# Kernel optimization log

Measured on AMD Instinct MI355X. Metric: run time of the kernel, lower is better.

The kernel has to match this reference:

```python
import jax, jax.numpy as jnp
import numpy as np

B, S, D, H = 2, 2048, 1024, 16
HD = D // H  # 64


def setup_inputs() -> dict:
    key = jax.random.key(0)
    ks = jax.random.split(key, 11)
    w_scale = 1.0 / np.sqrt(D)
    Q = jax.random.normal(ks[0], (B, S, D), jnp.float32)
    K = jax.random.normal(ks[1], (B, S, D), jnp.float32)
    V = jax.random.normal(ks[2], (B, S, D), jnp.float32)
    # causal mask: True = masked (matches torch masked_fill semantics)
    mask = ~jnp.tril(jnp.ones((S, S), bool))[None, None]  # [1,1,S,S]
    # RoPE freqs (precomputed cos/sin of freqs_cis, shape [S, HD//2])
    inv_freq = 1.0 / (10000.0 ** (jnp.arange(0, HD, 2, dtype=jnp.float32) / HD))
    angles = jnp.arange(S, dtype=jnp.float32)[:, None] * inv_freq[None, :]
    freqs_cos, freqs_sin = jnp.cos(angles), jnp.sin(angles)
    wq = jax.random.normal(ks[3], (D, D), jnp.float32) * w_scale
    wk = jax.random.normal(ks[4], (D, D), jnp.float32) * w_scale
    wv = jax.random.normal(ks[5], (D, D), jnp.float32) * w_scale
    wo = jax.random.normal(ks[6], (D, D), jnp.float32) * w_scale
    bq = jax.random.normal(ks[7], (D,), jnp.float32) * 0.01
    bk = jax.random.normal(ks[8], (D,), jnp.float32) * 0.01
    bv = jax.random.normal(ks[9], (D,), jnp.float32) * 0.01
    bo = jax.random.normal(ks[10], (D,), jnp.float32) * 0.01
    return {"Q": Q, "K": K, "V": V, "mask": mask,
            "freqs_cos": freqs_cos, "freqs_sin": freqs_sin,
            "wq": wq, "bq": bq, "wk": wk, "bk": bk,
            "wv": wv, "bv": bv, "wo": wo, "bo": bo}


def _rope(x, cos, sin):
    # x: [B,S,H,HD]; complex pairing of adjacent dims as in view_as_complex
    xr, xi = x[..., 0::2], x[..., 1::2]
    c = cos[None, :, None, :]
    s = sin[None, :, None, :]
    out_r = xr * c - xi * s
    out_i = xr * s + xi * c
    return jnp.stack([out_r, out_i], axis=-1).reshape(x.shape)


def reference(Q, K, V, mask, freqs_cos, freqs_sin, wq, bq, wk, bk, wv, bv, wo, bo):
    b, s, d = Q.shape
    h = H
    hd = d // h
    q = (Q @ wq.T + bq).reshape(b, s, h, hd)
    k = (K @ wk.T + bk).reshape(b, s, h, hd)
    v = (V @ wv.T + bv).reshape(b, s, h, hd)
    q = _rope(q, freqs_cos, freqs_sin)
    k = _rope(k, freqs_cos, freqs_sin)
    q = q.transpose(0, 2, 1, 3)  # [B,H,S,HD]
    k = k.transpose(0, 2, 1, 3)
    v = v.transpose(0, 2, 1, 3)
    scale = jnp.sqrt(jnp.float32(hd))
    energy = jnp.einsum('bhqd,bhkd->bhqk', q, k) / scale
    energy = jnp.where(mask, jnp.float32(-1e10), energy)
    attn = jax.nn.softmax(energy, axis=-1)  # dropout p=0.0 -> identity
    out = jnp.einsum('bhqk,bhkd->bhqd', attn, v)
    out = out.transpose(0, 2, 1, 3).reshape(b, s, d)
    return out @ wo.T + bo
```

## Files before the change

kernel.cpp:

```cpp
#include <hip/hip_runtime.h>
#include <stdint.h>

#define NB 2
#define NS 2048
#define ND 1024
#define NH 16
#define NHD 64
#define NM (NB*NS)

typedef __bf16 bf16;
typedef float f32x4 __attribute__((ext_vector_type(4)));
typedef __bf16 bf16x8 __attribute__((ext_vector_type(8)));
typedef __bf16 bf16x4 __attribute__((ext_vector_type(4)));

#define MFMA16(a,b,c) __builtin_amdgcn_mfma_f32_16x16x32_bf16(a,b,c,0,0,0)

__device__ __forceinline__ void gld_lds16(const bf16* g, bf16* l) {
  __builtin_amdgcn_global_load_lds((const __attribute__((address_space(1))) void*)g,
                                   (__attribute__((address_space(3))) void*)l,
                                   16, 0, 0);
}

__device__ __forceinline__ void block_sync_lds() {
  asm volatile("s_waitcnt lgkmcnt(0)\n\ts_barrier" ::: "memory");
}

__global__ __launch_bounds__(256)
void cvt3(const float* __restrict__ s0, const float* __restrict__ s1,
          const float* __restrict__ s2, bf16* __restrict__ dst, int n4each) {
  const int t = blockIdx.y;
  const float* s = (t == 0) ? s0 : (t == 1) ? s1 : s2;
  int i = blockIdx.x * blockDim.x + threadIdx.x;
  if (i >= n4each) return;
  float4 v = ((const float4*)s)[i];
  bf16x4 o = { (bf16)v.x, (bf16)v.y, (bf16)v.z, (bf16)v.w };
  ((bf16x4*)(dst + (size_t)t * n4each * 4))[i] = o;
}

__global__ __launch_bounds__(256)
void cvt_w4(const float* __restrict__ s0, const float* __restrict__ s1,
            const float* __restrict__ s2, const float* __restrict__ s3,
            bf16* __restrict__ dst, int n4each) {
  const int t = blockIdx.y;
  const float* s = (t == 0) ? s0 : (t == 1) ? s1 : (t == 2) ? s2 : s3;
  int i = blockIdx.x * blockDim.x + threadIdx.x;
  if (i >= n4each) return;
  float4 v = ((const float4*)s)[i];
  bf16x4 o = { (bf16)v.x, (bf16)v.y, (bf16)v.z, (bf16)v.w };
  ((bf16x4*)(dst + (size_t)t * n4each * 4))[i] = o;
}

template<int MODE>
__global__ __launch_bounds__(256)
void gemm_nt(const bf16* __restrict__ A, const bf16* __restrict__ W,
             const float* __restrict__ b0, const float* __restrict__ b1,
             const float* __restrict__ b2,
             const float* __restrict__ fc, const float* __restrict__ fs,
             bf16* __restrict__ obf, bf16* __restrict__ vtp,
             float* __restrict__ of) {
  constexpr int K = ND;
  constexpr int BN = (MODE == 0) ? 128 : 64;
  constexpr int NJ = (MODE == 0) ? 4 : 2;
  constexpr int ITB = (MODE == 0) ? 4 : 2;
  __shared__ __align__(16) bf16 As[128 * 64];
  __shared__ __align__(16) bf16 Bs[BN * 64];
  const int tid = threadIdx.x;
  const int w = tid >> 6, lane = tid & 63;

  const int id = blockIdx.x;
  const int xcd = id & 7, r = id >> 3;
  int t, nt, mt;
  if (MODE == 0) { t = r >> 5; const int rem = r & 31; nt = rem & 7;  mt = xcd + 8 * (rem >> 3); }
  else           { t = 0;                              nt = r & 15;   mt = xcd + 8 * (r >> 4);   }

  const bf16* Ab = A + (size_t)t * ((size_t)NM * K);
  const bf16* Wb = W + (size_t)t * ((size_t)ND * K);
  const float* bias = (t == 0) ? b0 : (t == 1) ? b1 : b2;
  const int wr = (w >> 1) * 64, wc = (w & 1) * (BN / 2);
  f32x4 acc[4][NJ] = {};

  const int swsrc = (((lane & 7) ^ ((lane >> 3) & 7)) << 3);
  const bf16* ga = Ab + (size_t)(mt * 128 + w * 8 + (lane >> 3)) * K + swsrc;
  const bf16* gb = Wb + (size_t)(nt * BN + w * 8 + (lane >> 3)) * K + swsrc;

  for (int k0 = 0; k0 < K; k0 += 64) {
    __syncthreads();
#pragma unroll
    for (int it = 0; it < 4; ++it)
      gld_lds16(ga + (size_t)(it * 32) * K + k0, As + (it * 4 + w) * 512);
#pragma unroll
    for (int it = 0; it < ITB; ++it)
      gld_lds16(gb + (size_t)(it * 32) * K + k0, Bs + (it * 4 + w) * 512);
    __syncthreads();

#pragma unroll
    for (int ks = 0; ks < 2; ++ks) {
      bf16x8 af[4], bfr[NJ];
#pragma unroll
      for (int i = 0; i < 4; ++i) {
        const int row = wr + i * 16 + (lane & 15);
        af[i] = *(const bf16x8*)&As[row * 64 +
                 (((ks * 4 + (lane >> 4)) ^ (lane & 7)) << 3)];
      }
#pragma unroll
      for (int j = 0; j < NJ; ++j) {
        const int row = wc + j * 16 + (lane & 15);
        bfr[j] = *(const bf16x8*)&Bs[row * 64 +
                  (((ks * 4 + (lane >> 4)) ^ (lane & 7)) << 3)];
      }
#pragma unroll
      for (int i = 0; i < 4; ++i)
#pragma unroll
        for (int j = 0; j < NJ; ++j)
          acc[i][j] = MFMA16(af[i], bfr[j], acc[i][j]);
    }
  }

#pragma unroll
  for (int i = 0; i < 4; ++i) {
#pragma unroll
    for (int j = 0; j < NJ; ++j) {
      const int gcol = nt * BN + wc + j * 16 + (lane & 15);
      const float bv = bias[gcol];
      if (MODE == 0 && t == 2) {
        const int s0g = mt * 128 + wr + i * 16 + (lane >> 4) * 4;
        const int b = s0g >> 11, s = s0g & (NS - 1);
        const int h = gcol >> 6, hd = gcol & 63;
        bf16x4 pk = { (bf16)(acc[i][j][0] + bv), (bf16)(acc[i][j][1] + bv),
                      (bf16)(acc[i][j][2] + bv), (bf16)(acc[i][j][3] + bv) };
        *(bf16x4*)&vtp[((size_t)(b * NH + h) * NHD + hd) * NS + s] = pk;
        continue;
      }
#pragma unroll
      for (int r4 = 0; r4 < 4; ++r4) {
        const int grow = mt * 128 + wr + i * 16 + (lane >> 4) * 4 + r4;
        float v = acc[i][j][r4] + bv;
        if (MODE == 0) {
          const int b = grow >> 11, s = grow & (NS - 1);
          const int h = gcol >> 6, hd = gcol & 63;
          float pv = __shfl_xor(v, 1);
          const int ii = hd >> 1;
          float c  = fc[(s << 5) + ii];
          float sn = fs[(s << 5) + ii];
          v = ((hd & 1) == 0) ? (v * c - pv * sn) : (pv * sn + v * c);
          if (t == 0) v *= 0.18033688011112042f;
          obf[(size_t)t * ((size_t)NM * ND) +
              (((size_t)(b * NH + h) * NS + s) * NHD + hd)] = (bf16)v;
        } else {
          of[(size_t)grow * ND + gcol] = v;
        }
      }
    }
  }
}

__device__ __forceinline__ void attn_tile(
    const bf16 (*__restrict__ Ksh)[72], const bf16 (*__restrict__ Vsh)[72],
    bf16 (*__restrict__ Pw)[72], const bf16x8* qf, f32x4* o,
    float& m, float& l, int qi, int kk0, bool diag, int qrow, int grp) {
  f32x4 sc[4] = {};
  __builtin_amdgcn_s_setprio(1);
#pragma unroll
  for (int ch = 0; ch < 2; ++ch)
#pragma unroll
    for (int cb = 0; cb < 4; ++cb) {
      bf16x8 kf = *(const bf16x8*)&Ksh[cb * 16 + qrow][ch * 32 + grp * 8];
      sc[cb] = MFMA16(kf, qf[ch], sc[cb]);
    }
  __builtin_amdgcn_s_setprio(0);

  if (diag) {
#pragma unroll
    for (int cb = 0; cb < 4; ++cb)
#pragma unroll
      for (int r = 0; r < 4; ++r)
        if (kk0 + cb * 16 + grp * 4 + r > qi) sc[cb][r] = -1e30f;
  }

  float pm = sc[0][0];
#pragma unroll
  for (int cb = 0; cb < 4; ++cb)
#pragma unroll
    for (int r = 0; r < 4; ++r) pm = fmaxf(pm, sc[cb][r]);
  pm = fmaxf(pm, __shfl_xor(pm, 16));
  pm = fmaxf(pm, __shfl_xor(pm, 32));
  const float mn = fmaxf(m, pm);
  const float scl = exp2f(m - mn);
  m = mn;
  l *= scl;
#pragma unroll
  for (int cb = 0; cb < 4; ++cb) {
    bf16x4 pk;
#pragma unroll
    for (int r = 0; r < 4; ++r) {
      float p = exp2f(sc[cb][r] - mn);
      l += p;
      pk[r] = (bf16)p;
    }
    *(bf16x4*)&Pw[qrow][cb * 16 + grp * 4] = pk;
  }
#pragma unroll
  for (int hb = 0; hb < 4; ++hb)
#pragma unroll
    for (int r = 0; r < 4; ++r) o[hb][r] *= scl;

  __builtin_amdgcn_s_setprio(1);
#pragma unroll
  for (int ch = 0; ch < 2; ++ch) {
    bf16x8 pa = *(const bf16x8*)&Pw[qrow][ch * 32 + grp * 8];
#pragma unroll
    for (int hb = 0; hb < 4; ++hb) {
      bf16x8 vf = *(const bf16x8*)&Vsh[hb * 16 + qrow][ch * 32 + grp * 8];
      o[hb] = MFMA16(vf, pa, o[hb]);
    }
  }
  __builtin_amdgcn_s_setprio(0);
}

__global__ __launch_bounds__(512, 4)
void attn_k(const bf16* __restrict__ q, const bf16* __restrict__ k,
            const bf16* __restrict__ vt, bf16* __restrict__ out) {
  __shared__ __align__(16) char smem[55296];
  auto Ks = (bf16(*)[64][72])smem;
  auto Vs = (bf16(*)[64][72])(smem + 18432);
  auto P  = (bf16(*)[16][72])(smem + 36864);
  auto MO = (float(*)[2][16][68])smem;
  auto ML = (float(*)[2][16][2])(smem + 36864);

  const int tid = threadIdx.x;
  const int w = tid >> 6, lane = tid & 63;
  const int h = w >> 2, wl = w & 3;
  const int qrow = lane & 15, grp = lane >> 4;
  const int bh = blockIdx.x, j = blockIdx.y;
  const int b = bh >> 4, hh = bh & (NH - 1);
  const int tA = j, tB = 31 - j;

  const bf16* qb = q + (size_t)bh * NS * NHD;
  const bf16* kb = k + (size_t)bh * NS * NHD;
  const bf16* vb = vt + (size_t)bh * NHD * NS;

  const int nA = (j >= h) ? (((j - h) >> 1) + 1) : 0;
  const int nB = (((31 - j) - h) >> 1) + 1;
  const int len = nA + nB;

  const int q0A = tA * 64 + wl * 16, q0B = tB * 64 + wl * 16;
  bf16x8 qfA[2], qfB[2];
#pragma unroll
  for (int ch = 0; ch < 2; ++ch) {
    qfA[ch] = *(const bf16x8*)&qb[(size_t)(q0A + qrow) * NHD + ch * 32 + grp * 8];
    qfB[ch] = *(const bf16x8*)&qb[(size_t)(q0B + qrow) * NHD + ch * 32 + grp * 8];
  }

  f32x4 oA[4] = {}, oB[4] = {};
  float mA = -1e30f, lA = 0.f, mB = -1e30f, lB = 0.f;

  const int local = tid & 255;
  const int r0 = local >> 3, c0 = (local & 7) * 8;

  bf16x8 ka0, ka1, va0, va1;
  auto load_round = [&](int r) {
    const bool isA = r < nA;
    const int kt = isA ? (h + 2 * r) : (h + 2 * (r - nA));
    const int kk0 = kt * 64;
    ka0 = *(const bf16x8*)&kb[(size_t)(kk0 + r0) * NHD + c0];
    ka1 = *(const bf16x8*)&kb[(size_t)(kk0 + r0 + 32) * NHD + c0];
    va0 = *(const bf16x8*)&vb[(size_t)r0 * NS + kk0 + c0];
    va1 = *(const bf16x8*)&vb[(size_t)(r0 + 32) * NS + kk0 + c0];
  };

  load_round(0);
  for (int r = 0; r < 17; ++r) {
    const bool act = r < len;
    if (act) {
      *(bf16x8*)&Ks[h][r0][c0]      = ka0;
      *(bf16x8*)&Ks[h][r0 + 32][c0] = ka1;
      *(bf16x8*)&Vs[h][r0][c0]      = va0;
      *(bf16x8*)&Vs[h][r0 + 32][c0] = va1;
    }
    block_sync_lds();
    const bool isA = r < nA;
    const int kt = isA ? (h + 2 * r) : (h + 2 * (r - nA));
    if (r + 1 < len) load_round(r + 1);
    if (act) {
      if (isA)
        attn_tile(Ks[h], Vs[h], P[w], qfA, oA, mA, lA,
                  q0A + qrow, kt * 64, kt == tA, qrow, grp);
      else
        attn_tile(Ks[h], Vs[h], P[w], qfB, oB, mB, lB,
                  q0B + qrow, kt * 64, kt == tB, qrow, grp);
    }
    block_sync_lds();
  }

  lA += __shfl_xor(lA, 16); lA += __shfl_xor(lA, 32);
  lB += __shfl_xor(lB, 16); lB += __shfl_xor(lB, 32);

  __syncthreads();

  if (h == 1) {
#pragma unroll
    for (int hb = 0; hb < 4; ++hb) {
      *(f32x4*)&MO[wl][0][qrow][hb * 16 + grp * 4] = oA[hb];
      *(f32x4*)&MO[wl][1][qrow][hb * 16 + grp * 4] = oB[hb];
    }
    if (grp == 0) {
      ML[wl][0][qrow][0] = mA; ML[wl][0][qrow][1] = lA;
      ML[wl][1][qrow][0] = mB; ML[wl][1][qrow][1] = lB;
    }
  }
  __syncthreads();

  if (h == 0) {
#pragma unroll
    for (int sub = 0; sub < 2; ++sub) {
      const float m0 = sub ? mB : mA, l0 = sub ? lB : lA;
      const f32x4* o0 = sub ? oB : oA;
      const float m1 = ML[wl][sub][qrow][0], l1 = ML[wl][sub][qrow][1];
      const float mm = fmaxf(m0, m1);
      const float s0 = exp2f(m0 - mm), s1 = exp2f(m1 - mm);
      const float inv = 1.f / (l0 * s0 + l1 * s1);
      const int s = (sub ? q0B : q0A) + qrow;
      bf16* op = out + (size_t)(b * NS + s) * ND + hh * NHD + grp * 4;
#pragma unroll
      for (int hb = 0; hb < 4; ++hb) {
        f32x4 o1 = *(const f32x4*)&MO[wl][sub][qrow][hb * 16 + grp * 4];
        bf16x4 ov = { (bf16)((o0[hb][0] * s0 + o1[0] * s1) * inv),
                      (bf16)((o0[hb][1] * s0 + o1[1] * s1) * inv),
                      (bf16)((o0[hb][2] * s0 + o1[2] * s1) * inv),
                      (bf16)((o0[hb][3] * s0 + o1[3] * s1) * inv) };
        *(bf16x4*)&op[hb * 16] = ov;
      }
    }
  }
}

extern "C" void kernel_launch(void* const* d_in, const int* in_sizes, int n_in,
                              void* d_out, int out_size, void* d_ws, size_t ws_size,
                              hipStream_t stream) {
  const float* Q  = (const float*)d_in[0];
  const float* K  = (const float*)d_in[1];
  const float* V  = (const float*)d_in[2];
  const float* fc = (const float*)d_in[4];
  const float* fs = (const float*)d_in[5];
  const float* wq = (const float*)d_in[6];
  const float* bq = (const float*)d_in[7];
  const float* wk = (const float*)d_in[8];
  const float* bk = (const float*)d_in[9];
  const float* wv = (const float*)d_in[10];
  const float* bv = (const float*)d_in[11];
  const float* wo = (const float*)d_in[12];
  const float* bo = (const float*)d_in[13];
  float* out = (float*)d_out;
  bf16* ws = (bf16*)d_ws;

  const size_t MB_ = 1024 * 1024;
  bf16* Qbf  = ws;
  bf16* Wqkv = ws + 12 * MB_;
  bf16* Wo   = ws + 15 * MB_;
  bf16* qp   = ws + 16 * MB_;
  bf16* vtp  = ws + 28 * MB_;
  bf16* aout = ws + 32 * MB_;
  bf16* kp   = ws + 20 * MB_;

  cvt3<<<dim3(4096, 3), 256, 0, stream>>>(Q, K, V, Qbf, 1048576);
  cvt_w4<<<dim3(1024, 4), 256, 0, stream>>>(wq, wk, wv, wo, Wqkv, 262144);

  gemm_nt<0><<<768, 256, 0, stream>>>(Qbf, Wqkv, bq, bk, bv, fc, fs,
                                      qp, vtp, nullptr);

  attn_k<<<dim3(32, 16), 512, 0, stream>>>(qp, kp, vtp, aout);

  gemm_nt<1><<<512, 256, 0, stream>>>(aout, Wo, bo, bo, bo, fc, fs,
                                      nullptr, nullptr, out);
}
```

Baseline: 126.3 us.

## Double-buffer attention K/V tiles with XOR-swizzled LDS and lazy softmax rescale

The attention kernel now double-buffers the K/V tiles in LDS. The next tile is stored and the one after is prefetched while the current one is computed, which drops one barrier per round. The padded [64][72] LDS layout is replaced by a 64-wide XOR-swizzled layout for K, V and P to avoid bank conflicts. The online softmax skips the max reduction and output rescale unless some row max grows by more than 8 (log2 units). LDS use grows from about 54 KB to 80 KB, which may cut occupancy below the 4 blocks per CU requested in the launch bounds.

```diff
diff --git a/kernel.cpp b/kernel.cpp
--- a/kernel.cpp
+++ b/kernel.cpp
@@ -155,16 +155,18 @@
 }
 
 __device__ __forceinline__ void attn_tile(
-    const bf16 (*__restrict__ Ksh)[72], const bf16 (*__restrict__ Vsh)[72],
-    bf16 (*__restrict__ Pw)[72], const bf16x8* qf, f32x4* o,
+    const bf16* __restrict__ Ksh, const bf16* __restrict__ Vsh,
+    bf16* __restrict__ Pw, const bf16x8* qf, f32x4* o,
     float& m, float& l, int qi, int kk0, bool diag, int qrow, int grp) {
+  const int s7 = qrow & 7;
   f32x4 sc[4] = {};
   __builtin_amdgcn_s_setprio(1);
 #pragma unroll
   for (int ch = 0; ch < 2; ++ch)
 #pragma unroll
     for (int cb = 0; cb < 4; ++cb) {
-      bf16x8 kf = *(const bf16x8*)&Ksh[cb * 16 + qrow][ch * 32 + grp * 8];
+      bf16x8 kf = *(const bf16x8*)
+        &Ksh[(cb * 16 + qrow) * 64 + (((ch * 4 + grp) ^ s7) << 3)];
       sc[cb] = MFMA16(kf, qf[ch], sc[cb]);
     }
   __builtin_amdgcn_s_setprio(0);
@@ -177,40 +179,47 @@
         if (kk0 + cb * 16 + grp * 4 + r > qi) sc[cb][r] = -1e30f;
   }
 
-  float pm = sc[0][0];
-#pragma unroll
-  for (int cb = 0; cb < 4; ++cb)
-#pragma unroll
-    for (int r = 0; r < 4; ++r) pm = fmaxf(pm, sc[cb][r]);
-  pm = fmaxf(pm, __shfl_xor(pm, 16));
-  pm = fmaxf(pm, __shfl_xor(pm, 32));
-  const float mn = fmaxf(m, pm);
-  const float scl = exp2f(m - mn);
-  m = mn;
-  l *= scl;
+  float a0 = fmaxf(fmaxf(sc[0][0], sc[0][1]), fmaxf(sc[0][2], sc[0][3]));
+  float a1 = fmaxf(fmaxf(sc[1][0], sc[1][1]), fmaxf(sc[1][2], sc[1][3]));
+  float a2 = fmaxf(fmaxf(sc[2][0], sc[2][1]), fmaxf(sc[2][2], sc[2][3]));
+  float a3 = fmaxf(fmaxf(sc[3][0], sc[3][1]), fmaxf(sc[3][2], sc[3][3]));
+  float pm = fmaxf(fmaxf(a0, a1), fmaxf(a2, a3));
+
+  if (__any(pm > m + 8.f)) {
+    float px = fmaxf(pm, __shfl_xor(pm, 16));
+    px = fmaxf(px, __shfl_xor(px, 32));
+    const float mn = fmaxf(m, px);
+    const float scl = exp2f(m - mn);
+    m = mn;
+    l *= scl;
+#pragma unroll
+    for (int hb = 0; hb < 4; ++hb)
+#pragma unroll
+      for (int r = 0; r < 4; ++r) o[hb][r] *= scl;
+  }
+
 #pragma unroll
   for (int cb = 0; cb < 4; ++cb) {
     bf16x4 pk;
 #pragma unroll
     for (int r = 0; r < 4; ++r) {
-      float p = exp2f(sc[cb][r] - mn);
+      float p = exp2f(sc[cb][r] - m);
       l += p;
       pk[r] = (bf16)p;
     }
-    *(bf16x4*)&Pw[qrow][cb * 16 + grp * 4] = pk;
-  }
-#pragma unroll
-  for (int hb = 0; hb < 4; ++hb)
-#pragma unroll
-    for (int r = 0; r < 4; ++r) o[hb][r] *= scl;
+    *(bf16x4*)&Pw[qrow * 64 + (((((cb << 1) | (grp >> 1)) ^ s7) << 3)) +
+                  ((grp & 1) << 2)] = pk;
+  }
 
   __builtin_amdgcn_s_setprio(1);
 #pragma unroll
   for (int ch = 0; ch < 2; ++ch) {
-    bf16x8 pa = *(const bf16x8*)&Pw[qrow][ch * 32 + grp * 8];
+    bf16x8 pa = *(const bf16x8*)
+      &Pw[qrow * 64 + (((ch * 4 + grp) ^ s7) << 3)];
 #pragma unroll
     for (int hb = 0; hb < 4; ++hb) {
-      bf16x8 vf = *(const bf16x8*)&Vsh[hb * 16 + qrow][ch * 32 + grp * 8];
+      bf16x8 vf = *(const bf16x8*)
+        &Vsh[(hb * 16 + qrow) * 64 + (((ch * 4 + grp) ^ s7) << 3)];
       o[hb] = MFMA16(vf, pa, o[hb]);
     }
   }
@@ -220,10 +229,9 @@
 __global__ __launch_bounds__(512, 4)
 void attn_k(const bf16* __restrict__ q, const bf16* __restrict__ k,
             const bf16* __restrict__ vt, bf16* __restrict__ out) {
-  __shared__ __align__(16) char smem[55296];
-  auto Ks = (bf16(*)[64][72])smem;
-  auto Vs = (bf16(*)[64][72])(smem + 18432);
-  auto P  = (bf16(*)[16][72])(smem + 36864);
+  __shared__ __align__(16) char smem[81920];
+  bf16* KV = (bf16*)smem;
+  bf16* Pr = (bf16*)(smem + 65536);
   auto MO = (float(*)[2][16][68])smem;
   auto ML = (float(*)[2][16][2])(smem + 36864);
 
@@ -255,7 +263,13 @@
   float mA = -1e30f, lA = 0.f, mB = -1e30f, lB = 0.f;
 
   const int local = tid & 255;
-  const int r0 = local >> 3, c0 = (local & 7) * 8;
+  const int r0 = local >> 3;
+  const int c0 = (local & 7) * 8;
+  const int sw = (((local & 7) ^ (r0 & 7)) << 3);
+
+  bf16* Pw = Pr + w * 1024;
+  auto Kb = [&](int buf) { return KV + ((h * 2 + buf) * 2 + 0) * 4096; };
+  auto Vb = [&](int buf) { return KV + ((h * 2 + buf) * 2 + 1) * 4096; };
 
   bf16x8 ka0, ka1, va0, va1;
   auto load_round = [&](int r) {
@@ -267,26 +281,33 @@
     va0 = *(const bf16x8*)&vb[(size_t)r0 * NS + kk0 + c0];
     va1 = *(const bf16x8*)&vb[(size_t)(r0 + 32) * NS + kk0 + c0];
   };
+  auto store_tile = [&](int buf) {
+    bf16* Ksc = Kb(buf);
+    bf16* Vsc = Vb(buf);
+    *(bf16x8*)&Ksc[r0 * 64 + sw]        = ka0;
+    *(bf16x8*)&Ksc[(r0 + 32) * 64 + sw] = ka1;
+    *(bf16x8*)&Vsc[r0 * 64 + sw]        = va0;
+    *(bf16x8*)&Vsc[(r0 + 32) * 64 + sw] = va1;
+  };
 
   load_round(0);
+  store_tile(0);
+  load_round(1);
+  block_sync_lds();
+
   for (int r = 0; r < 17; ++r) {
+    const int cur = r & 1;
     const bool act = r < len;
+    if (r + 1 < len) store_tile(cur ^ 1);
+    if (r + 2 < len) load_round(r + 2);
     if (act) {
-      *(bf16x8*)&Ks[h][r0][c0]      = ka0;
-      *(bf16x8*)&Ks[h][r0 + 32][c0] = ka1;
-      *(bf16x8*)&Vs[h][r0][c0]      = va0;
-      *(bf16x8*)&Vs[h][r0 + 32][c0] = va1;
-    }
-    block_sync_lds();
-    const bool isA = r < nA;
-    const int kt = isA ? (h + 2 * r) : (h + 2 * (r - nA));
-    if (r + 1 < len) load_round(r + 1);
-    if (act) {
+      const bool isA = r < nA;
+      const int kt = isA ? (h + 2 * r) : (h + 2 * (r - nA));
       if (isA)
-        attn_tile(Ks[h], Vs[h], P[w], qfA, oA, mA, lA,
+        attn_tile(Kb(cur), Vb(cur), Pw, qfA, oA, mA, lA,
                   q0A + qrow, kt * 64, kt == tA, qrow, grp);
       else
-        attn_tile(Ks[h], Vs[h], P[w], qfB, oB, mB, lB,
+        attn_tile(Kb(cur), Vb(cur), Pw, qfB, oB, mB, lB,
                   q0B + qrow, kt * 64, kt == tB, qrow, grp);
     }
     block_sync_lds();
@@ -358,9 +379,9 @@
   bf16* Wqkv = ws + 12 * MB_;
   bf16* Wo   = ws + 15 * MB_;
   bf16* qp   = ws + 16 * MB_;
+  bf16* kp   = ws + 20 * MB_;
   bf16* vtp  = ws + 28 * MB_;
   bf16* aout = ws + 32 * MB_;
-  bf16* kp   = ws + 20 * MB_;
 
   cvt3<<<dim3(4096, 3), 256, 0, stream>>>(Q, K, V, Qbf, 1048576);
   cvt_w4<<<dim3(1024, 4), 256, 0, stream>>>(wq, wk, wv, wo, Wqkv, 262144);
```

Measured after the change: 122.2 us. 1.03x faster.
